# Kernel optimization log

Hardware: AMD Instinct MI355X
Metric: run time of the kernel (lower is better)

Reference implementation:

```python
import jax, jax.numpy as jnp
import numpy as np

B, CIN, HW = 32, 64, 56
K, KS, STRIDE, PAD = 128, 3, 1, 1


def setup_inputs() -> dict:
    key = jax.random.key(0)
    kx, kw, kb = jax.random.split(key, 3)
    x = jax.random.normal(kx, (B, CIN, HW, HW), dtype=jnp.float32)
    weight = jax.random.normal(kw, (K, CIN, KS, KS), dtype=jnp.float32)
    offset = jax.random.normal(kb, (K, 1, 1), dtype=jnp.float32)
    return {"x": x, "weight": weight, "offset": offset}


def reference(x, weight, offset):
    # conv2d (NCHW, OIHW) with stride/padding, then add per-kernel scalar offset.
    # Equivalent to the module's im2col (create_window_column_matrix) + matmul
    # + reshape, plus self.offset broadcast over (B, K, s, s).
    out = jax.lax.conv_general_dilated(
        x, weight,
        window_strides=(STRIDE, STRIDE),
        padding=[(PAD, PAD), (PAD, PAD)],
        dimension_numbers=("NCHW", "OIHW", "NCHW"),
    )
    return out + offset  # offset (K,1,1) broadcasts against (B,K,s,s)
```

## Files before the change

kernel.cpp:

```cpp
#include <hip/hip_runtime.h>
#include <hip/hip_bf16.h>

namespace {

using frag_t    = __attribute__((ext_vector_type(8))) short;
using f32x4     = __attribute__((ext_vector_type(4))) float;
using float4_t  = __attribute__((ext_vector_type(4))) float;

constexpr int BATCH = 32;
constexpr int CIN   = 64;
constexpr int HWD   = 56;
constexpr int KOUT  = 128;
constexpr int SP    = HWD * HWD;
constexpr int KD    = 9 * CIN;
constexpr int BN    = 128;
constexpr int HALO  = 57;
constexpr int NEXT  = BN + 2 * HALO;
constexpr int NTILES= SP / BN + 1;
constexpr int TT    = BATCH * (SP / 64);
constexpr int WB    = (KOUT * KD + 255) / 256;

__device__ inline unsigned short f2bf(float f) {
    __hip_bfloat16 h = __float2bfloat16(f);
    return __builtin_bit_cast(unsigned short, h);
}

__global__ __launch_bounds__(256)
void prep_kernel(const float* __restrict__ x, const float* __restrict__ w,
                 unsigned short* __restrict__ wpA, unsigned short* __restrict__ xT)
{
    if (blockIdx.x >= TT) {
        const int idx = (blockIdx.x - TT) * 256 + threadIdx.x;
        if (idx < KOUT * KD) {
            const int kout = idx / KD, kk = idx - kout * KD;
            const int kc = kk >> 5, e = kk & 31;
            const int t = kk >> 6, c = kk & 63;
            const int ky = t / 3, kx = t - ky * 3;
            wpA[(kc * KOUT + kout) * 32 + e] = f2bf(w[((kout * CIN + c) * 3 + ky) * 3 + kx]);
        }
        return;
    }
    __shared__ float ls[64][68];
    const int bb   = blockIdx.x / (SP / 64);
    const int tile = blockIdx.x - bb * (SP / 64);
    const int sp0  = tile * 64;
    const int tid  = threadIdx.x;
    const int cq   = tid >> 4;
    const int spo  = (tid & 15) * 4;
    const float* xb = x + (size_t)bb * CIN * SP;
    #pragma unroll
    for (int j = 0; j < 4; ++j) {
        const int c = cq + 16 * j;
        float4_t v = *(const float4_t*)&xb[(size_t)c * SP + sp0 + spo];
        ls[spo + 0][c] = v.x; ls[spo + 1][c] = v.y;
        ls[spo + 2][c] = v.z; ls[spo + 3][c] = v.w;
    }
    __syncthreads();
    unsigned short* xo = xT + (size_t)(bb * SP + sp0) * 64;
    #pragma unroll
    for (int j = 0; j < 2; ++j) {
        const int s  = tid + 256 * j;
        const int sp = s >> 3, e = s & 7;
        frag_t u;
        #pragma unroll
        for (int q = 0; q < 8; ++q)
            u[q] = (short)f2bf(ls[sp][e * 8 + q]);
        *(frag_t*)&xo[sp * 64 + e * 8] = u;
    }
}

__global__ __launch_bounds__(256, 2)
void conv_mfma(const unsigned short* __restrict__ xT, const unsigned short* __restrict__ wpA,
               const float* __restrict__ off, float* __restrict__ out)
{
    __shared__ unsigned short xs[NEXT * 64];

    const int b    = blockIdx.y;
    const int sp0  = blockIdx.x * BN;
    const int tid  = threadIdx.x;
    const int lane = tid & 63;
    const int wid  = tid >> 6;

    {
        const unsigned short* xb = xT + (size_t)b * SP * 64;
        #pragma unroll
        for (int it = 0; it < 8; ++it) {
            const int s = it * 256 + tid;
            if (s < NEXT * 8) {
                const int r = s >> 3, e = s & 7;
                int g = sp0 - HALO + r;
                g = min(max(g, 0), SP - 1);
                frag_t v = *(const frag_t*)&xb[(size_t)g * 64 + e * 8];
                *(frag_t*)&xs[r * 64 + ((e * 8) ^ ((r & 7) << 3))] = v;
            }
        }
    }
    __syncthreads();

    const int wm  = (wid >> 1) * 64;
    const int wn  = (wid & 1) * 64;
    const int l15 = lane & 15;
    const int l4  = lane >> 4;

    unsigned long long mbits = 0ull;
    #pragma unroll
    for (int t = 0; t < 9; ++t) {
        const int dy = t / 3 - 1, dx = t % 3 - 1;
        #pragma unroll
        for (int nf = 0; nf < 4; ++nf) {
            const int sp = sp0 + wn + nf * 16 + l15;
            const int y  = sp / HWD;
            const int xc = sp - y * HWD;
            const bool v = ((unsigned)(y + dy) < (unsigned)HWD) &
                           ((unsigned)(xc + dx) < (unsigned)HWD);
            mbits |= (unsigned long long)(v ? 1 : 0) << (t * 4 + nf);
        }
    }

    const unsigned short* abase = wpA + (wm + l15) * 32 + 8 * l4;

    f32x4 acc[4][4] = {};
    const frag_t zf = {0,0,0,0,0,0,0,0};
    const int cread = 8 * l4;

    #pragma unroll
    for (int kc = 0; kc < 18; ++kc) {
        const int t  = kc >> 1;
        const int c0 = (kc & 1) * 32;
        const int s    = (t / 3 - 1) * HWD + (t % 3 - 1);
        const int row0 = wn + l15 + HALO + s;
        const int sw   = (row0 & 7) << 3;
        frag_t a[4], bfr[4];
        #pragma unroll
        for (int mi = 0; mi < 4; ++mi)
            a[mi] = *(const frag_t*)(abase + kc * (KOUT * 32) + mi * (16 * 32));
        #pragma unroll
        for (int nf = 0; nf < 4; ++nf) {
            const frag_t bl = *(const frag_t*)&xs[(row0 + 16 * nf) * 64
                                                 + ((c0 + cread) ^ sw)];
            const bool v = (mbits >> (t * 4 + nf)) & 1;
            bfr[nf] = v ? bl : zf;
        }
        #pragma unroll
        for (int mi = 0; mi < 4; ++mi)
            #pragma unroll
            for (int nf = 0; nf < 4; ++nf)
                acc[mi][nf] = __builtin_amdgcn_mfma_f32_16x16x32_bf16(
                    a[mi], bfr[nf], acc[mi][nf], 0, 0, 0);
    }

    const int spn = sp0 + wn + l15;
    #pragma unroll
    for (int mi = 0; mi < 4; ++mi) {
        const int km = wm + 16 * mi + 4 * l4;
        #pragma unroll
        for (int reg = 0; reg < 4; ++reg) {
            const int  kk  = km + reg;
            const float ofv = off[kk];
            float* ob = out + (size_t)(b * KOUT + kk) * SP;
            #pragma unroll
            for (int nf = 0; nf < 4; ++nf) {
                const int sp = spn + 16 * nf;
                if (sp < SP) ob[sp] = acc[mi][nf][reg] + ofv;
            }
        }
    }
}

__global__ __launch_bounds__(256)
void conv3x3_kernel(const float* __restrict__ x, const float* __restrict__ w,
                    const float* __restrict__ off, float* __restrict__ out)
{
    const int s  = blockIdx.x * 256 + threadIdx.x;
    const int b  = s / SP;
    const int sp = s - b * SP;
    const int y  = sp / HWD;
    const int xx = sp - y * HWD;
    const int k0 = blockIdx.y * 4;

    const int   xm1 = (xx > 0) ? xx - 1 : 0;
    const int   xp1 = (xx < HWD - 1) ? xx + 1 : HWD - 1;
    const float m0  = (xx > 0) ? 1.f : 0.f;
    const float m2  = (xx < HWD - 1) ? 1.f : 0.f;

    int ro[3]; float msk[3][3];
    #pragma unroll
    for (int ky = 0; ky < 3; ++ky) {
        const int  yy = y + ky - 1;
        const bool ok = (unsigned)yy < (unsigned)HWD;
        const float rm = ok ? 1.f : 0.f;
        ro[ky] = (ok ? yy : 0) * HWD;
        msk[ky][0] = rm * m0; msk[ky][1] = rm; msk[ky][2] = rm * m2;
    }
    float acc[4] = {0.f, 0.f, 0.f, 0.f};
    const float* xb = x + (size_t)b * CIN * SP;
    for (int c = 0; c < CIN; ++c) {
        const float* xc = xb + (size_t)c * SP;
        #pragma unroll
        for (int ky = 0; ky < 3; ++ky) {
            const float* xr = xc + ro[ky];
            const float v0 = xr[xm1] * msk[ky][0];
            const float v1 = xr[xx]  * msk[ky][1];
            const float v2 = xr[xp1] * msk[ky][2];
            const int wi = c * 9 + ky * 3;
            #pragma unroll
            for (int kk = 0; kk < 4; ++kk) {
                const float* wr = w + (size_t)(k0 + kk) * (CIN * 9) + wi;
                acc[kk] = fmaf(v0, wr[0], acc[kk]);
                acc[kk] = fmaf(v1, wr[1], acc[kk]);
                acc[kk] = fmaf(v2, wr[2], acc[kk]);
            }
        }
    }
    #pragma unroll
    for (int kk = 0; kk < 4; ++kk)
        out[(size_t)(b * KOUT + k0 + kk) * SP + sp] = acc[kk] + off[k0 + kk];
}

}

extern "C" void kernel_launch(void* const* d_in, const int* in_sizes, int n_in,
                              void* d_out, int out_size, void* d_ws, size_t ws_size,
                              hipStream_t stream)
{
    const float* x   = (const float*)d_in[0];
    const float* w   = (const float*)d_in[1];
    const float* off = (const float*)d_in[2];
    float* out = (float*)d_out;

    const size_t wpa_bytes = (size_t)KOUT * KD * 2;
    const size_t xt_bytes  = (size_t)BATCH * SP * CIN * 2;

    if (ws_size >= wpa_bytes + xt_bytes) {
        unsigned short* wpA = (unsigned short*)d_ws;
        unsigned short* xT  = (unsigned short*)((char*)d_ws + wpa_bytes);
        prep_kernel<<<TT + WB, 256, 0, stream>>>(x, w, wpA, xT);
        dim3 grid(NTILES, BATCH);
        conv_mfma<<<grid, dim3(256, 1, 1), 0, stream>>>(xT, wpA, off, out);
    } else {
        dim3 grid((BATCH * SP) / 256, KOUT / 4);
        conv3x3_kernel<<<grid, dim3(256, 1, 1), 0, stream>>>(x, w, off, out);
    }
}
```

Baseline: 45.16 us.

## Software-pipeline A/B fragment loads and remap workgroups across XCDs

The MFMA loop now prefetches weight fragments two k-chunks ahead and LDS input fragments one chunk ahead, so global and LDS load latency overlaps the matrix instructions. The grid is flattened to 1D and block ids are permuted so consecutive dispatched blocks, which land on different XCDs, map to contiguous spatial tiles within a batch, aiming for better L2 locality of halo data. The deeper prefetch raises VGPR pressure, which could hurt occupancy under launch_bounds(256,2). NWG (29*32=928) is divisible by 8, so the permutation is a bijection.

```diff
diff --git a/kernel.cpp b/kernel.cpp
--- a/kernel.cpp
+++ b/kernel.cpp
@@ -17,6 +17,7 @@
 constexpr int HALO  = 57;
 constexpr int NEXT  = BN + 2 * HALO;
 constexpr int NTILES= SP / BN + 1;
+constexpr int NWG   = NTILES * BATCH;
 constexpr int TT    = BATCH * (SP / 64);
 constexpr int WB    = (KOUT * KD + 255) / 256;
 
@@ -75,8 +76,10 @@
 {
     __shared__ unsigned short xs[NEXT * 64];
 
-    const int b    = blockIdx.y;
-    const int sp0  = blockIdx.x * BN;
+    const int d    = blockIdx.x;
+    const int wk   = (d & 7) * (NWG / 8) + (d >> 3);
+    const int b    = wk / NTILES;
+    const int sp0  = (wk - b * NTILES) * BN;
     const int tid  = threadIdx.x;
     const int lane = tid & 63;
     const int wid  = tid >> 6;
@@ -118,35 +121,49 @@
     }
 
     const unsigned short* abase = wpA + (wm + l15) * 32 + 8 * l4;
-
-    f32x4 acc[4][4] = {};
+    const int cread = 8 * l4;
     const frag_t zf = {0,0,0,0,0,0,0,0};
-    const int cread = 8 * l4;
-
-    #pragma unroll
-    for (int kc = 0; kc < 18; ++kc) {
+
+    auto load_a = [&](frag_t dst[4], int kc) {
+        #pragma unroll
+        for (int mi = 0; mi < 4; ++mi)
+            dst[mi] = *(const frag_t*)(abase + kc * (KOUT * 32) + mi * (16 * 32));
+    };
+    auto load_b = [&](frag_t dst[4], int kc) {
         const int t  = kc >> 1;
         const int c0 = (kc & 1) * 32;
         const int s    = (t / 3 - 1) * HWD + (t % 3 - 1);
         const int row0 = wn + l15 + HALO + s;
         const int sw   = (row0 & 7) << 3;
-        frag_t a[4], bfr[4];
-        #pragma unroll
-        for (int mi = 0; mi < 4; ++mi)
-            a[mi] = *(const frag_t*)(abase + kc * (KOUT * 32) + mi * (16 * 32));
         #pragma unroll
         for (int nf = 0; nf < 4; ++nf) {
             const frag_t bl = *(const frag_t*)&xs[(row0 + 16 * nf) * 64
                                                  + ((c0 + cread) ^ sw)];
-            const bool v = (mbits >> (t * 4 + nf)) & 1;
-            bfr[nf] = v ? bl : zf;
-        }
+            dst[nf] = ((mbits >> (t * 4 + nf)) & 1) ? bl : zf;
+        }
+    };
+
+    f32x4 acc[4][4] = {};
+    frag_t a0[4], a1[4], bP[4];
+    load_a(a0, 0);
+    load_a(a1, 1);
+    load_b(bP, 0);
+
+    #pragma unroll
+    for (int kc = 0; kc < 18; ++kc) {
+        frag_t aC[4], bC[4];
+        #pragma unroll
+        for (int mi = 0; mi < 4; ++mi) { aC[mi] = a0[mi]; a0[mi] = a1[mi]; }
+        #pragma unroll
+        for (int nf = 0; nf < 4; ++nf) { bC[nf] = bP[nf]; }
+        if (kc + 2 < 18) load_a(a1, kc + 2);
+        if (kc + 1 < 18) load_b(bP, kc + 1);
         #pragma unroll
         for (int mi = 0; mi < 4; ++mi)
             #pragma unroll
             for (int nf = 0; nf < 4; ++nf)
                 acc[mi][nf] = __builtin_amdgcn_mfma_f32_16x16x32_bf16(
-                    a[mi], bfr[nf], acc[mi][nf], 0, 0, 0);
+                    aC[mi], bC[nf], acc[mi][nf], 0, 0, 0);
     }
 
     const int spn = sp0 + wn + l15;
@@ -235,8 +252,7 @@
         unsigned short* wpA = (unsigned short*)d_ws;
         unsigned short* xT  = (unsigned short*)((char*)d_ws + wpa_bytes);
         prep_kernel<<<TT + WB, 256, 0, stream>>>(x, w, wpA, xT);
-        dim3 grid(NTILES, BATCH);
-        conv_mfma<<<grid, dim3(256, 1, 1), 0, stream>>>(xT, wpA, off, out);
+        conv_mfma<<<NWG, dim3(256, 1, 1), 0, stream>>>(xT, wpA, off, out);
     } else {
         dim3 grid((BATCH * SP) / 256, KOUT / 4);
         conv3x3_kernel<<<grid, dim3(256, 1, 1), 0, stream>>>(x, w, off, out);
```

New measurement: 44.11 us. 1.02x faster.

## Split output channels across two workgroups, use direct global-to-LDS loads, remap blocks

Applied to the files above, without the earlier changes.

Each conv workgroup now computes half of the 128 output channels, which doubles the grid and halves the accumulator registers so occupancy can rise to 4 blocks per CU. The halo tile is staged with global_load_lds, writing straight into shared memory with a per-lane swizzle instead of going through registers. A blockIdx remap spreads consecutive blocks across XCDs, aiming to keep the two channel-halves and neighbouring tiles of a batch together for L2 reuse. The cost is that the input tile is loaded twice, once per channel half.

```diff
diff --git a/kernel.cpp b/kernel.cpp
--- a/kernel.cpp
+++ b/kernel.cpp
@@ -17,6 +17,7 @@
 constexpr int HALO  = 57;
 constexpr int NEXT  = BN + 2 * HALO;
 constexpr int NTILES= SP / BN + 1;
+constexpr int NWG2  = NTILES * BATCH * 2;
 constexpr int TT    = BATCH * (SP / 64);
 constexpr int WB    = (KOUT * KD + 255) / 256;
 
@@ -69,35 +70,44 @@
     }
 }
 
-__global__ __launch_bounds__(256, 2)
+__global__ __launch_bounds__(256, 4)
 void conv_mfma(const unsigned short* __restrict__ xT, const unsigned short* __restrict__ wpA,
                const float* __restrict__ off, float* __restrict__ out)
 {
     __shared__ unsigned short xs[NEXT * 64];
 
-    const int b    = blockIdx.y;
-    const int sp0  = blockIdx.x * BN;
+    const int d    = blockIdx.x;
+    const int wk   = (d & 7) * (NWG2 / 8) + (d >> 3);
+    const int kh   = wk & 1;
+    const int wk2  = wk >> 1;
+    const int b    = wk2 / NTILES;
+    const int sp0  = (wk2 - b * NTILES) * BN;
     const int tid  = threadIdx.x;
     const int lane = tid & 63;
     const int wid  = tid >> 6;
 
     {
         const unsigned short* xb = xT + (size_t)b * SP * 64;
+        const int lsw = ((lane & 7) * 8) ^ ((lane >> 3) << 3);
         #pragma unroll
         for (int it = 0; it < 8; ++it) {
-            const int s = it * 256 + tid;
-            if (s < NEXT * 8) {
-                const int r = s >> 3, e = s & 7;
+            const int R0 = it * 32 + wid * 8;
+            const int r  = R0 + (lane >> 3);
+            if (r < NEXT) {
                 int g = sp0 - HALO + r;
                 g = min(max(g, 0), SP - 1);
-                frag_t v = *(const frag_t*)&xb[(size_t)g * 64 + e * 8];
-                *(frag_t*)&xs[r * 64 + ((e * 8) ^ ((r & 7) << 3))] = v;
+                const unsigned short* src = xb + (size_t)g * 64 + lsw;
+                __builtin_amdgcn_global_load_lds(
+                    (const __attribute__((address_space(1))) unsigned int*)src,
+                    (__attribute__((address_space(3))) unsigned int*)&xs[R0 * 64 + (lane) * 8],
+                    16, 0, 0);
             }
         }
     }
+    asm volatile("s_waitcnt vmcnt(0)" ::: "memory");
     __syncthreads();
 
-    const int wm  = (wid >> 1) * 64;
+    const int wmL = (wid >> 1) * 32;
     const int wn  = (wid & 1) * 64;
     const int l15 = lane & 15;
     const int l4  = lane >> 4;
@@ -117,11 +127,11 @@
         }
     }
 
-    const unsigned short* abase = wpA + (wm + l15) * 32 + 8 * l4;
-
-    f32x4 acc[4][4] = {};
+    const unsigned short* abase = wpA + (size_t)(kh * 64 + wmL + l15) * 32 + 8 * l4;
+    const int cread = 8 * l4;
     const frag_t zf = {0,0,0,0,0,0,0,0};
-    const int cread = 8 * l4;
+
+    f32x4 acc[2][4] = {};
 
     #pragma unroll
     for (int kc = 0; kc < 18; ++kc) {
@@ -130,19 +140,18 @@
         const int s    = (t / 3 - 1) * HWD + (t % 3 - 1);
         const int row0 = wn + l15 + HALO + s;
         const int sw   = (row0 & 7) << 3;
-        frag_t a[4], bfr[4];
-        #pragma unroll
-        for (int mi = 0; mi < 4; ++mi)
-            a[mi] = *(const frag_t*)(abase + kc * (KOUT * 32) + mi * (16 * 32));
+        frag_t a[2], bfr[4];
+        #pragma unroll
+        for (int mi = 0; mi < 2; ++mi)
+            a[mi] = *(const frag_t*)(abase + (size_t)(kc * KOUT + mi * 16) * 32);
         #pragma unroll
         for (int nf = 0; nf < 4; ++nf) {
             const frag_t bl = *(const frag_t*)&xs[(row0 + 16 * nf) * 64
                                                  + ((c0 + cread) ^ sw)];
-            const bool v = (mbits >> (t * 4 + nf)) & 1;
-            bfr[nf] = v ? bl : zf;
-        }
-        #pragma unroll
-        for (int mi = 0; mi < 4; ++mi)
+            bfr[nf] = ((mbits >> (t * 4 + nf)) & 1) ? bl : zf;
+        }
+        #pragma unroll
+        for (int mi = 0; mi < 2; ++mi)
             #pragma unroll
             for (int nf = 0; nf < 4; ++nf)
                 acc[mi][nf] = __builtin_amdgcn_mfma_f32_16x16x32_bf16(
@@ -151,8 +160,8 @@
 
     const int spn = sp0 + wn + l15;
     #pragma unroll
-    for (int mi = 0; mi < 4; ++mi) {
-        const int km = wm + 16 * mi + 4 * l4;
+    for (int mi = 0; mi < 2; ++mi) {
+        const int km = kh * 64 + wmL + 16 * mi + 4 * l4;
         #pragma unroll
         for (int reg = 0; reg < 4; ++reg) {
             const int  kk  = km + reg;
@@ -235,8 +244,7 @@
         unsigned short* wpA = (unsigned short*)d_ws;
         unsigned short* xT  = (unsigned short*)((char*)d_ws + wpa_bytes);
         prep_kernel<<<TT + WB, 256, 0, stream>>>(x, w, wpA, xT);
-        dim3 grid(NTILES, BATCH);
-        conv_mfma<<<grid, dim3(256, 1, 1), 0, stream>>>(xT, wpA, off, out);
+        conv_mfma<<<NWG2, dim3(256, 1, 1), 0, stream>>>(xT, wpA, off, out);
     } else {
         dim3 grid((BATCH * SP) / 256, KOUT / 4);
         conv3x3_kernel<<<grid, dim3(256, 1, 1), 0, stream>>>(x, w, off, out);
```

Measured after the change: 43.72 us. 1.03x faster.

## Fuse input transpose and bf16 conversion into the MFMA conv kernel

Applied to the files above, without the earlier changes.

Drops the separate prep pass that wrote a bf16 channel-last copy of x to workspace. Each conv workgroup now loads fp32 NCHW tiles, including halo, transposes them through LDS and converts them to bf16 itself. This removes a global write and re-read of the transformed input. In exchange, halo rows are loaded and converted redundantly by neighbouring tiles, and the load phase adds extra syncs. The change also remaps block indices to spread work across XCDs and raises the occupancy hint to 3.

```diff
diff --git a/kernel.cpp b/kernel.cpp
--- a/kernel.cpp
+++ b/kernel.cpp
@@ -15,9 +15,9 @@
 constexpr int KD    = 9 * CIN;
 constexpr int BN    = 128;
 constexpr int HALO  = 57;
-constexpr int NEXT  = BN + 2 * HALO;
+constexpr int NST   = 256;
 constexpr int NTILES= SP / BN + 1;
-constexpr int TT    = BATCH * (SP / 64);
+constexpr int NWG   = NTILES * BATCH;
 constexpr int WB    = (KOUT * KD + 255) / 256;
 
 __device__ inline unsigned short f2bf(float f) {
@@ -26,76 +26,71 @@
 }
 
 __global__ __launch_bounds__(256)
-void prep_kernel(const float* __restrict__ x, const float* __restrict__ w,
-                 unsigned short* __restrict__ wpA, unsigned short* __restrict__ xT)
-{
-    if (blockIdx.x >= TT) {
-        const int idx = (blockIdx.x - TT) * 256 + threadIdx.x;
-        if (idx < KOUT * KD) {
-            const int kout = idx / KD, kk = idx - kout * KD;
-            const int kc = kk >> 5, e = kk & 31;
-            const int t = kk >> 6, c = kk & 63;
-            const int ky = t / 3, kx = t - ky * 3;
-            wpA[(kc * KOUT + kout) * 32 + e] = f2bf(w[((kout * CIN + c) * 3 + ky) * 3 + kx]);
-        }
-        return;
-    }
-    __shared__ float ls[64][68];
-    const int bb   = blockIdx.x / (SP / 64);
-    const int tile = blockIdx.x - bb * (SP / 64);
-    const int sp0  = tile * 64;
-    const int tid  = threadIdx.x;
-    const int cq   = tid >> 4;
-    const int spo  = (tid & 15) * 4;
-    const float* xb = x + (size_t)bb * CIN * SP;
-    #pragma unroll
-    for (int j = 0; j < 4; ++j) {
-        const int c = cq + 16 * j;
-        float4_t v = *(const float4_t*)&xb[(size_t)c * SP + sp0 + spo];
-        ls[spo + 0][c] = v.x; ls[spo + 1][c] = v.y;
-        ls[spo + 2][c] = v.z; ls[spo + 3][c] = v.w;
-    }
-    __syncthreads();
-    unsigned short* xo = xT + (size_t)(bb * SP + sp0) * 64;
-    #pragma unroll
-    for (int j = 0; j < 2; ++j) {
-        const int s  = tid + 256 * j;
-        const int sp = s >> 3, e = s & 7;
-        frag_t u;
-        #pragma unroll
-        for (int q = 0; q < 8; ++q)
-            u[q] = (short)f2bf(ls[sp][e * 8 + q]);
-        *(frag_t*)&xo[sp * 64 + e * 8] = u;
-    }
-}
-
-__global__ __launch_bounds__(256, 2)
-void conv_mfma(const unsigned short* __restrict__ xT, const unsigned short* __restrict__ wpA,
-               const float* __restrict__ off, float* __restrict__ out)
-{
-    __shared__ unsigned short xs[NEXT * 64];
-
-    const int b    = blockIdx.y;
-    const int sp0  = blockIdx.x * BN;
+void wconv_kernel(const float* __restrict__ w, unsigned short* __restrict__ wpA)
+{
+    const int idx = blockIdx.x * 256 + threadIdx.x;
+    if (idx < KOUT * KD) {
+        const int kout = idx / KD, kk = idx - kout * KD;
+        const int kc = kk >> 5, e = kk & 31;
+        const int t = kk >> 6, c = kk & 63;
+        const int ky = t / 3, kx = t - ky * 3;
+        wpA[(kc * KOUT + kout) * 32 + e] = f2bf(w[((kout * CIN + c) * 3 + ky) * 3 + kx]);
+    }
+}
+
+__global__ __launch_bounds__(256, 3)
+void conv_fused(const float* __restrict__ x, const unsigned short* __restrict__ wpA,
+                const float* __restrict__ off, float* __restrict__ out)
+{
+    __shared__ unsigned short xs[NST * 64];
+    __shared__ float ls[64][65];
+
+    const int d    = blockIdx.x;
+    const int wk   = (d & 7) * (NWG / 8) + (d >> 3);
+    const int b    = wk / NTILES;
+    const int sp0  = (wk - b * NTILES) * BN;
     const int tid  = threadIdx.x;
     const int lane = tid & 63;
     const int wid  = tid >> 6;
 
     {
-        const unsigned short* xb = xT + (size_t)b * SP * 64;
-        #pragma unroll
-        for (int it = 0; it < 8; ++it) {
-            const int s = it * 256 + tid;
-            if (s < NEXT * 8) {
-                const int r = s >> 3, e = s & 7;
-                int g = sp0 - HALO + r;
-                g = min(max(g, 0), SP - 1);
-                frag_t v = *(const frag_t*)&xb[(size_t)g * 64 + e * 8];
-                *(frag_t*)&xs[r * 64 + ((e * 8) ^ ((r & 7) << 3))] = v;
-            }
-        }
-    }
-    __syncthreads();
+        const float* xb  = x + (size_t)b * CIN * SP;
+        const int    spo = (tid & 15) * 4;
+        const int    cb  = tid >> 4;
+        for (int s4 = 0; s4 < 4; ++s4) {
+            const int g0 = sp0 - HALO + s4 * 64 + spo;
+            #pragma unroll
+            for (int j = 0; j < 4; ++j) {
+                const int c = cb + 16 * j;
+                const float* xc = xb + (size_t)c * SP;
+                float4_t v;
+                if (g0 >= 0 && g0 + 3 < SP) {
+                    v = *(const float4_t*)&xc[g0];
+                } else {
+                    #pragma unroll
+                    for (int k2 = 0; k2 < 4; ++k2) {
+                        int g = g0 + k2; g = min(max(g, 0), SP - 1);
+                        v[k2] = xc[g];
+                    }
+                }
+                ls[spo + 0][c] = v.x; ls[spo + 1][c] = v.y;
+                ls[spo + 2][c] = v.z; ls[spo + 3][c] = v.w;
+            }
+            __syncthreads();
+            #pragma unroll
+            for (int j = 0; j < 2; ++j) {
+                const int t2 = tid + 256 * j;
+                const int sp = t2 >> 3, e = t2 & 7;
+                frag_t u;
+                #pragma unroll
+                for (int q = 0; q < 8; ++q)
+                    u[q] = (short)f2bf(ls[sp][e * 8 + q]);
+                const int spg = s4 * 64 + sp;
+                *(frag_t*)&xs[spg * 64 + ((e * 8) ^ ((spg & 7) << 3))] = u;
+            }
+            __syncthreads();
+        }
+    }
 
     const int wm  = (wid >> 1) * 64;
     const int wn  = (wid & 1) * 64;
@@ -103,25 +98,29 @@
     const int l4  = lane >> 4;
 
     unsigned long long mbits = 0ull;
+    int yv[4], xv[4];
+    #pragma unroll
+    for (int nf = 0; nf < 4; ++nf) {
+        const int sp = sp0 + wn + nf * 16 + l15;
+        yv[nf] = sp / HWD;
+        xv[nf] = sp - yv[nf] * HWD;
+    }
     #pragma unroll
     for (int t = 0; t < 9; ++t) {
         const int dy = t / 3 - 1, dx = t % 3 - 1;
         #pragma unroll
         for (int nf = 0; nf < 4; ++nf) {
-            const int sp = sp0 + wn + nf * 16 + l15;
-            const int y  = sp / HWD;
-            const int xc = sp - y * HWD;
-            const bool v = ((unsigned)(y + dy) < (unsigned)HWD) &
-                           ((unsigned)(xc + dx) < (unsigned)HWD);
+            const bool v = ((unsigned)(yv[nf] + dy) < (unsigned)HWD) &
+                           ((unsigned)(xv[nf] + dx) < (unsigned)HWD);
             mbits |= (unsigned long long)(v ? 1 : 0) << (t * 4 + nf);
         }
     }
 
-    const unsigned short* abase = wpA + (wm + l15) * 32 + 8 * l4;
+    const unsigned short* abase = wpA + (size_t)(wm + l15) * 32 + 8 * l4;
+    const int cread = 8 * l4;
+    const frag_t zf = {0,0,0,0,0,0,0,0};
 
     f32x4 acc[4][4] = {};
-    const frag_t zf = {0,0,0,0,0,0,0,0};
-    const int cread = 8 * l4;
 
     #pragma unroll
     for (int kc = 0; kc < 18; ++kc) {
@@ -133,13 +132,12 @@
         frag_t a[4], bfr[4];
         #pragma unroll
         for (int mi = 0; mi < 4; ++mi)
-            a[mi] = *(const frag_t*)(abase + kc * (KOUT * 32) + mi * (16 * 32));
+            a[mi] = *(const frag_t*)(abase + (size_t)(kc * KOUT + mi * 16) * 32);
         #pragma unroll
         for (int nf = 0; nf < 4; ++nf) {
             const frag_t bl = *(const frag_t*)&xs[(row0 + 16 * nf) * 64
                                                  + ((c0 + cread) ^ sw)];
-            const bool v = (mbits >> (t * 4 + nf)) & 1;
-            bfr[nf] = v ? bl : zf;
+            bfr[nf] = ((mbits >> (t * 4 + nf)) & 1) ? bl : zf;
         }
         #pragma unroll
         for (int mi = 0; mi < 4; ++mi)
@@ -229,14 +227,11 @@
     float* out = (float*)d_out;
 
     const size_t wpa_bytes = (size_t)KOUT * KD * 2;
-    const size_t xt_bytes  = (size_t)BATCH * SP * CIN * 2;
-
-    if (ws_size >= wpa_bytes + xt_bytes) {
+
+    if (ws_size >= wpa_bytes) {
         unsigned short* wpA = (unsigned short*)d_ws;
-        unsigned short* xT  = (unsigned short*)((char*)d_ws + wpa_bytes);
-        prep_kernel<<<TT + WB, 256, 0, stream>>>(x, w, wpA, xT);
-        dim3 grid(NTILES, BATCH);
-        conv_mfma<<<grid, dim3(256, 1, 1), 0, stream>>>(xT, wpA, off, out);
+        wconv_kernel<<<WB, 256, 0, stream>>>(w, wpA);
+        conv_fused<<<NWG, dim3(256, 1, 1), 0, stream>>>(x, wpA, off, out);
     } else {
         dim3 grid((BATCH * SP) / 256, KOUT / 4);
         conv3x3_kernel<<<grid, dim3(256, 1, 1), 0, stream>>>(x, w, off, out);
```

Measured after the change: 58.30 us. +29.1%, slower.
